# Performance work log

Hardware: AMD Instinct MI355X
Metric: run time of the kernel (lower is better)

Reference implementation:

```python
import jax, jax.numpy as jnp
import numpy as np

B, T, K = 128, 4096, 64
START, STOP = 62, 63
NEG = -10000.0


def setup_inputs() -> dict:
    key = jax.random.key(0)
    k1, k2, k3 = jax.random.split(key, 3)
    feats = jax.random.normal(k1, (B, T, K), dtype=jnp.float32)
    # gold tags never include START/STOP
    tags = jax.random.randint(k2, (B, T), 0, START)
    transitions = jax.random.normal(k3, (K, K), dtype=jnp.float32)
    # mirror the torch __init__ masking: no transition INTO start, none OUT of stop
    transitions = transitions.at[START, :].set(NEG).at[:, STOP].set(NEG)
    return {"feats": feats, "tags": tags, "transitions": transitions}


def _crf_single(feats, tags, transitions):
    """feats: [T,K], tags: [T], transitions: [K,K] (trans[next, prev])."""
    init = jnp.full((K,), NEG, dtype=feats.dtype).at[START].set(0.0)

    # ---- forward algorithm (log partition), vectorized over the tag loop ----
    def fwd_step(alpha, feat):
        # alpha[i] + trans[j, i] + feat[j]  ->  logsumexp over prev i
        new = jax.nn.logsumexp(alpha[None, :] + transitions, axis=1) + feat
        return new, None

    alpha, _ = jax.lax.scan(fwd_step, init, feats)
    forward_score = jax.nn.logsumexp(alpha + transitions[STOP])

    # ---- gold path score (_score_session) ----
    prev_tags = jnp.concatenate([jnp.array([START], dtype=tags.dtype), tags[:-1]])
    emit = jnp.take_along_axis(feats, tags[:, None], axis=1)[:, 0]  # feats[t, tags[t]]
    gold_score = jnp.sum(transitions[tags, prev_tags] + emit) + transitions[STOP, tags[-1]]

    nll = forward_score - gold_score  # neg_log_likelihood

    # ---- Viterbi decode ----
    def vit_step(delta, feat):
        scores = delta[None, :] + transitions  # [next, prev]
        bp = jnp.argmax(scores, axis=1)
        new = jnp.max(scores, axis=1) + feat  # feat added after argmax, as in torch
        return new, bp

    delta, bps = jax.lax.scan(vit_step, init, feats)  # bps: [T, K]
    terminal = delta + transitions[STOP]
    best_last = jnp.argmax(terminal)
    path_score = terminal[best_last]

    def back_step(tag, bp_t):
        return bp_t[tag], tag

    _, best_path = jax.lax.scan(back_step, best_last, bps, reverse=True)  # [T]
    return nll, path_score, best_path


def reference(feats, tags, transitions):
    nll, path_score, best_path = jax.vmap(_crf_single, in_axes=(0, 0, None))(
        feats, tags, transitions
    )
    return nll, path_score, best_path
```

## Files before the change

### kernel.cpp

```cpp
#include <hip/hip_runtime.h>

namespace {
constexpr int Tn = 4096;
constexpr int Kn = 64;
constexpr int BATCH = 128;
constexpr int START_TAG = 62;
constexpr int STOP_TAG = 63;
constexpr float NEGV = -10000.0f;
constexpr int CH = 64;
constexpr int NCH = Tn / CH;
constexpr int GL = 8;
constexpr int NG = Tn / GL;
constexpr int RS = 128;
constexpr int RB = 128;
constexpr int CW = 16;

__device__ __forceinline__ float rfl(float x) {
    return __uint_as_float(__builtin_amdgcn_readfirstlane(__float_as_uint(x)));
}
__device__ __forceinline__ void cfence() { __asm__ volatile("" ::: "memory"); }
__device__ __forceinline__ void lgkm0() { __asm__ volatile("s_waitcnt lgkmcnt(0)" ::: "memory"); }
__device__ __forceinline__ int imin(int a, int b) { return a < b ? a : b; }
__device__ __forceinline__ float m3(float a, float b, float c) {
    return fmaxf(fmaxf(a, b), c);
}

__global__ __launch_bounds__(256, 1)
void crf_kernel(const float* __restrict__ feats,
                const int* __restrict__ tags,
                const float* __restrict__ trans,
                float* __restrict__ out,
                unsigned int* __restrict__ bp32)
{
    const int tid = threadIdx.x;
    const int lane = tid & 63;
    const int wid = tid >> 6;
    const int b = blockIdx.x & (BATCH - 1);
    const size_t fb = (size_t)b * Tn * Kn;

    __shared__ float gw[4];
    __shared__ __align__(16) float vbuf[Kn];
    __shared__ __align__(16) float ring_v[RS][Kn];
    __shared__ float ring_m[RS][Kn];
    __shared__ unsigned char ring_bp[RB][Kn];
    __shared__ unsigned char snap[NCH * Kn];
    __shared__ unsigned char echain[NCH];
    __shared__ int prog_a[Kn], prog_b[Kn], prog_c[Kn], prog_d[Kn];
    __shared__ int done_b[Kn], done_c[Kn];

#define GATHER16(BASE) do {                                                    \
        const float4* vp_ = (const float4*)(BASE);                             \
        g0 = vp_[0];  g1 = vp_[1];  g2 = vp_[2];  g3 = vp_[3];                 \
        g4 = vp_[4];  g5 = vp_[5];  g6 = vp_[6];  g7 = vp_[7];                 \
        g8 = vp_[8];  g9 = vp_[9];  g10 = vp_[10]; g11 = vp_[11];              \
        g12 = vp_[12]; g13 = vp_[13]; g14 = vp_[14]; g15 = vp_[15];            \
    } while (0)

    if (blockIdx.x < BATCH) {
        float gold = 0.0f;
        {
            const int t0 = tid * (Tn / 256);
            int prev = (tid == 0) ? START_TAG : tags[(size_t)b * Tn + t0 - 1];
            for (int k = 0; k < Tn / 256; ++k) {
                const int t = t0 + k;
                const int tg = tags[(size_t)b * Tn + t];
                gold += trans[tg * Kn + prev] + feats[fb + (size_t)t * Kn + tg];
                prev = tg;
            }
            if (tid == 255) gold += trans[STOP_TAG * Kn + prev];
            #pragma unroll
            for (int off = 32; off; off >>= 1) gold += __shfl_down(gold, off);
            if (lane == 0) gw[wid] = gold;
        }
        __syncthreads();
        if (wid != 0) return;

        float ES[Kn];
        #pragma unroll
        for (int q = 0; q < Kn / 4; ++q) {
            const float4 t4 = ((const float4*)(trans + lane * Kn))[q];
            ES[4*q+0] = __expf(t4.x); ES[4*q+1] = __expf(t4.y);
            ES[4*q+2] = __expf(t4.z); ES[4*q+3] = __expf(t4.w);
        }
        float v = (lane == START_TAG) ? 1.0f : 0.0f;
        float O = 0.0f;
        float fc[GL], fn[GL], Fc[GL];
        #pragma unroll
        for (int k = 0; k < GL; ++k) fc[k] = feats[fb + (size_t)k * Kn + lane];

        float4 g0, g1, g2, g3, g4, g5, g6, g7, g8, g9, g10, g11, g12, g13, g14, g15;
        vbuf[lane] = v;
        GATHER16(vbuf);

#define FMAQ(Q, A, B2, C, D) ({                                                \
        float s0_ = 0.f, s1_ = 0.f, s2_ = 0.f, s3_ = 0.f;                      \
        s0_ = fmaf(ES[16*(Q)+0],  (A).x,  s0_); s1_ = fmaf(ES[16*(Q)+1],  (A).y,  s1_); \
        s2_ = fmaf(ES[16*(Q)+2],  (A).z,  s2_); s3_ = fmaf(ES[16*(Q)+3],  (A).w,  s3_); \
        s0_ = fmaf(ES[16*(Q)+4],  (B2).x, s0_); s1_ = fmaf(ES[16*(Q)+5],  (B2).y, s1_); \
        s2_ = fmaf(ES[16*(Q)+6],  (B2).z, s2_); s3_ = fmaf(ES[16*(Q)+7],  (B2).w, s3_); \
        s0_ = fmaf(ES[16*(Q)+8],  (C).x,  s0_); s1_ = fmaf(ES[16*(Q)+9],  (C).y,  s1_); \
        s2_ = fmaf(ES[16*(Q)+10], (C).z,  s2_); s3_ = fmaf(ES[16*(Q)+11], (C).w,  s3_); \
        s0_ = fmaf(ES[16*(Q)+12], (D).x,  s0_); s1_ = fmaf(ES[16*(Q)+13], (D).y,  s1_); \
        s2_ = fmaf(ES[16*(Q)+14], (D).z,  s2_); s3_ = fmaf(ES[16*(Q)+15], (D).w,  s3_); \
        (s0_ + s1_) + (s2_ + s3_); })

#define FWD_STEP(K) do {                                                       \
        const float w0_ = FMAQ(0, g0,  g1,  g2,  g3);                          \
        const float w1_ = FMAQ(1, g4,  g5,  g6,  g7);                          \
        const float w2_ = FMAQ(2, g8,  g9,  g10, g11);                         \
        const float w3_ = FMAQ(3, g12, g13, g14, g15);                         \
        const float w_ = ((w0_ + w1_) + (w2_ + w3_)) * Fc[K];                  \
        const float wz_ = rfl(w_);                                             \
        v = w_ * __builtin_amdgcn_rcpf(wz_);                                   \
        vbuf[lane] = v;                                                        \
        GATHER16(vbuf);                 \
        O += __logf(wz_);                   \
    } while (0)

        for (int g = 0; g < NG; ++g) {
            if (g + 1 < NG) {
                const size_t base = fb + (size_t)(g + 1) * GL * Kn + lane;
                #pragma unroll
                for (int k = 0; k < GL; ++k) fn[k] = feats[base + (size_t)k * Kn];
            }
            #pragma unroll
            for (int k = 0; k < GL; ++k) Fc[k] = __expf(fc[k]);
            #pragma unroll
            for (int k = 0; k < GL; ++k) FWD_STEP(k);
            #pragma unroll
            for (int k = 0; k < GL; ++k) fc[k] = fn[k];
        }
#undef FWD_STEP
        {
            const float a = O + __logf(v);
            const float x = a + trans[STOP_TAG * Kn + lane];
            float mx = x;
            #pragma unroll
            for (int off = 32; off; off >>= 1) mx = fmaxf(mx, __shfl_xor(mx, off));
            float se = __expf(x - mx);
            #pragma unroll
            for (int off = 32; off; off >>= 1) se += __shfl_xor(se, off);
            if (lane == 0)
                out[b] = (mx + __logf(se)) - (((gw[0] + gw[1]) + (gw[2] + gw[3])));
        }
        return;
    }

    volatile int* pa = (volatile int*)prog_a;
    volatile int* pb = (volatile int*)prog_b;
    volatile int* pc = (volatile int*)prog_c;
    volatile int* pd = (volatile int*)prog_d;
    volatile int* db = (volatile int*)done_b;
    volatile int* dc = (volatile int*)done_c;
    if (wid == 0) { pa[lane] = 0; pb[lane] = 0; }
    if (wid == 1) { pc[lane] = 0; pd[lane] = 0; }
    if (wid == 2) { db[lane] = 0; dc[lane] = 0; }
    __syncthreads();

    float trS[Kn];
    #pragma unroll
    for (int q = 0; q < Kn / 4; ++q) {
        const float4 t4 = ((const float4*)(trans + lane * Kn))[q];
        trS[4*q+0] = t4.x; trS[4*q+1] = t4.y; trS[4*q+2] = t4.z; trS[4*q+3] = t4.w;
    }

    if (wid == 0) {
        float v = (lane == START_TAG) ? 0.0f : NEGV;
        float fc[GL], fn[GL];
        #pragma unroll
        for (int k = 0; k < GL; ++k) fc[k] = feats[fb + (size_t)k * Kn + lane];

        float4 g0, g1, g2, g3, g4, g5, g6, g7, g8, g9, g10, g11, g12, g13, g14, g15;
        ring_v[0][lane] = v;
        GATHER16(ring_v[0]);

#define VQ(Q, DV) ({                                                           \
        const float sx_ = (DV).x + trS[4*(Q)+0];                               \
        const float sy_ = (DV).y + trS[4*(Q)+1];                               \
        const float sz_ = (DV).z + trS[4*(Q)+2];                               \
        const float sw_ = (DV).w + trS[4*(Q)+3];                               \
        fmaxf(m3(sx_, sy_, sz_), sw_); })

#define VIT_STEP(K) do {                                                       \
        const int t_ = g * GL + (K);                                           \
        const float q0_  = VQ(0,  g0),  q1_  = VQ(1,  g1);                     \
        const float q2_  = VQ(2,  g2),  q3_  = VQ(3,  g3);                     \
        const float q4_  = VQ(4,  g4),  q5_  = VQ(5,  g5);                     \
        const float q6_  = VQ(6,  g6),  q7_  = VQ(7,  g7);                     \
        const float q8_  = VQ(8,  g8),  q9_  = VQ(9,  g9);                     \
        const float q10_ = VQ(10, g10), q11_ = VQ(11, g11);                    \
        const float q12_ = VQ(12, g12), q13_ = VQ(13, g13);                    \
        const float q14_ = VQ(14, g14), q15_ = VQ(15, g15);                    \
        const float r0_ = m3(q0_,  q1_,  q2_);                                 \
        const float r1_ = m3(q3_,  q4_,  q5_);                                 \
        const float r2_ = m3(q6_,  q7_,  q8_);                                 \
        const float r3_ = m3(q9_,  q10_, q11_);                                \
        const float r4_ = m3(q12_, q13_, q14_);                                \
        const float mm_ = fmaxf(m3(m3(r0_, r1_, r2_), r3_, r4_), q15_);        \
        v = mm_ + fc[K];                 \
        float* nb_ = ring_v[(t_ + 1) & (RS - 1)];                              \
        nb_[lane] = v;                                                         \
        GATHER16(nb_);                   \
        ring_m[t_ & (RS - 1)][lane] = mm_;             \
    } while (0)

        for (int g = 0; g < NG; ++g) {
            if (g + 1 < NG) {
                const size_t base = fb + (size_t)(g + 1) * GL * Kn + lane;
                #pragma unroll
                for (int k = 0; k < GL; ++k) fn[k] = feats[base + (size_t)k * Kn];
            }
            if ((g & 3) == 0 && g >= 16) {
                const int t0 = g * GL;
                cfence();
                while (pb[lane] < t0 - 88 || pc[lane] < t0 - 88)
                    __builtin_amdgcn_s_sleep(1);
                cfence();
            }
            #pragma unroll
            for (int k = 0; k < GL; ++k) VIT_STEP(k);
            cfence();
            pa[lane] = g * GL + GL;
            #pragma unroll
            for (int k = 0; k < GL; ++k) fc[k] = fn[k];
        }
#undef VIT_STEP
#undef VQ
        const float term = v + trans[STOP_TAG * Kn + lane];
        float bv = term;
        int bi = lane;
        #pragma unroll
        for (int off = 32; off; off >>= 1) {
            const float ov = __shfl_xor(bv, off);
            const int oi = __shfl_xor(bi, off);
            if (ov > bv || (ov == bv && oi < bi)) { bv = ov; bi = oi; }
        }
        if (lane == 0) out[BATCH + b] = bv;
        while (pd[lane] < Tn) __builtin_amdgcn_s_sleep(1);
        cfence();
        if (lane == 0) {
            int e = bi;
            for (int c = NCH - 1; c >= 0; --c) {
                echain[c] = (unsigned char)e;
                e = snap[c * Kn + e];
            }
        }
        lgkm0();
        while (db[lane] == 0 || dc[lane] == 0) __builtin_amdgcn_s_sleep(1);
        cfence();
        int tag = echain[lane];
        float* po = out + 2 * BATCH + (size_t)b * Tn;
        const size_t dwb = (size_t)b * (Tn / 4);
        for (int k = CH - 1; k >= 0; --k) {
            const int t = lane * CH + k;
            po[t] = (float)tag;
            tag = (int)((bp32[(dwb + (size_t)(t >> 2)) * Kn + tag] >> (8 * (t & 3))) & 63u);
        }
    } else if (wid == 1 || wid == 2) {
        const int par = wid - 1;
        const size_t dwb = (size_t)b * (Tn / 4);
        volatile int* my = (par == 0) ? pb : pc;
        for (int c0 = par * CW; c0 < Tn; c0 += 2 * CW) {
            while (pa[lane] < c0 + CW) __builtin_amdgcn_s_sleep(1);
            cfence();
            if (c0 >= RB) {
                while (pd[lane] < c0 - (RB - CW)) __builtin_amdgcn_s_sleep(1);
                cfence();
            }
            for (int k4 = 0; k4 < CW; k4 += 4) {
                unsigned int bp4 = 0;
                #pragma unroll
                for (int k = 0; k < 4; ++k) {
                    const int t = c0 + k4 + k;
                    const float4* vp = (const float4*)ring_v[t & (RS - 1)];
                    const float m = ring_m[t & (RS - 1)][lane];
                    int qi[16];
                    #pragma unroll
                    for (int q = 0; q < 16; ++q) {
                        const float4 dv = vp[q];
                        const float sx = dv.x + trS[4*q+0];
                        const float sy = dv.y + trS[4*q+1];
                        const float sz = dv.z + trS[4*q+2];
                        const float sw = dv.w + trS[4*q+3];
                        const int ix = (sx == m) ? 4*q+0 : 255;
                        const int iy = (sy == m) ? 4*q+1 : 255;
                        const int iz = (sz == m) ? 4*q+2 : 255;
                        const int iw = (sw == m) ? 4*q+3 : 255;
                        qi[q] = imin(imin(ix, iy), imin(iz, iw));
                    }
                    int i8[8];
                    #pragma unroll
                    for (int q = 0; q < 8; ++q) i8[q] = imin(qi[2*q], qi[2*q+1]);
                    const int idx = imin(imin(imin(i8[0], i8[1]), imin(i8[2], i8[3])),
                                         imin(imin(i8[4], i8[5]), imin(i8[6], i8[7])));
                    ring_bp[t & (RB - 1)][lane] = (unsigned char)idx;
                    bp4 |= (unsigned int)idx << (8 * k);
                }
                bp32[(dwb + (size_t)((c0 + k4) >> 2)) * Kn + lane] = bp4;
            }
            cfence();
            my[lane] = c0 + CW;
        }
        __asm__ volatile("s_waitcnt vmcnt(0)" ::: "memory");
        if (par == 0) db[lane] = 1; else dc[lane] = 1;
    } else {
        int h = lane;
        for (int c0 = 0; c0 < Tn; c0 += CW) {
            volatile int* pp = ((c0 >> 4) & 1) ? pc : pb;
            while (pp[lane] < c0 + CW) __builtin_amdgcn_s_sleep(1);
            cfence();
            int bpv[CW];
            #pragma unroll
            for (int k = 0; k < CW; ++k)
                bpv[k] = (int)ring_bp[(c0 + k) & (RB - 1)][lane];
            #pragma unroll
            for (int k = 0; k < CW; ++k) h = __shfl(h, bpv[k]);
            if (((c0 >> 4) & 3) == 3) {
                snap[(c0 >> 6) * Kn + lane] = (unsigned char)h;
                h = lane;
            }
            cfence();
            pd[lane] = c0 + CW;
        }
    }
#undef GATHER16
#undef FMAQ
}
}

extern "C" void kernel_launch(void* const* d_in, const int* in_sizes, int n_in,
                              void* d_out, int out_size, void* d_ws, size_t ws_size,
                              hipStream_t stream)
{
    const float* feats = (const float*)d_in[0];
    const int* tags   = (const int*)d_in[1];
    const float* trans = (const float*)d_in[2];
    float* out = (float*)d_out;
    unsigned int* bp = (unsigned int*)d_ws;
    hipLaunchKernelGGL(crf_kernel, dim3(2 * BATCH), dim3(256), 0, stream,
                       feats, tags, trans, out, bp);
}
```

Before: 1.684 ms.

## Broadcast recurrence state via readlane and tree-compose backpointer shuffles

The forward and Viterbi recurrences no longer write the 64-wide state vector to LDS and read it back as 16 float4s each step. Each lane now pulls the previous-step values straight from registers with v_readlane, removing an LDS store/load round trip from the serial critical path; the price is 64 readlanes per step plus possible VALU-to-readlane hazard stalls. The backtrace wave also stops applying 16 chained shuffles to h. It composes the 16 backpointer maps in a pairwise tree first, so the serial shuffle chain is only a few levels deep. Viterbi still writes ring_v and ring_m for the other waves, and the ring_m store is moved earlier.

```diff
diff --git a/kernel.cpp b/kernel.cpp
--- a/kernel.cpp
+++ b/kernel.cpp
@@ -25,6 +25,8 @@
     return fmaxf(fmaxf(a, b), c);
 }
 
+#define RLV(I) __int_as_float(__builtin_amdgcn_readlane(vi_, (I)))
+
 __global__ __launch_bounds__(256, 1)
 void crf_kernel(const float* __restrict__ feats,
                 const int* __restrict__ tags,
@@ -39,22 +41,13 @@
     const size_t fb = (size_t)b * Tn * Kn;
 
     __shared__ float gw[4];
-    __shared__ __align__(16) float vbuf[Kn];
     __shared__ __align__(16) float ring_v[RS][Kn];
-    __shared__ float ring_m[RS][Kn];
+    __shared__ __align__(16) float ring_m[RS][Kn];
     __shared__ unsigned char ring_bp[RB][Kn];
     __shared__ unsigned char snap[NCH * Kn];
     __shared__ unsigned char echain[NCH];
     __shared__ int prog_a[Kn], prog_b[Kn], prog_c[Kn], prog_d[Kn];
     __shared__ int done_b[Kn], done_c[Kn];
-
-#define GATHER16(BASE) do {                                                    \
-        const float4* vp_ = (const float4*)(BASE);                             \
-        g0 = vp_[0];  g1 = vp_[1];  g2 = vp_[2];  g3 = vp_[3];                 \
-        g4 = vp_[4];  g5 = vp_[5];  g6 = vp_[6];  g7 = vp_[7];                 \
-        g8 = vp_[8];  g9 = vp_[9];  g10 = vp_[10]; g11 = vp_[11];              \
-        g12 = vp_[12]; g13 = vp_[13]; g14 = vp_[14]; g15 = vp_[15];            \
-    } while (0)
 
     if (blockIdx.x < BATCH) {
         float gold = 0.0f;
@@ -88,33 +81,36 @@
         #pragma unroll
         for (int k = 0; k < GL; ++k) fc[k] = feats[fb + (size_t)k * Kn + lane];
 
-        float4 g0, g1, g2, g3, g4, g5, g6, g7, g8, g9, g10, g11, g12, g13, g14, g15;
-        vbuf[lane] = v;
-        GATHER16(vbuf);
-
-#define FMAQ(Q, A, B2, C, D) ({                                                \
+#define FMAQ_RL(Q) ({                                                          \
         float s0_ = 0.f, s1_ = 0.f, s2_ = 0.f, s3_ = 0.f;                      \
-        s0_ = fmaf(ES[16*(Q)+0],  (A).x,  s0_); s1_ = fmaf(ES[16*(Q)+1],  (A).y,  s1_); \
-        s2_ = fmaf(ES[16*(Q)+2],  (A).z,  s2_); s3_ = fmaf(ES[16*(Q)+3],  (A).w,  s3_); \
-        s0_ = fmaf(ES[16*(Q)+4],  (B2).x, s0_); s1_ = fmaf(ES[16*(Q)+5],  (B2).y, s1_); \
-        s2_ = fmaf(ES[16*(Q)+6],  (B2).z, s2_); s3_ = fmaf(ES[16*(Q)+7],  (B2).w, s3_); \
-        s0_ = fmaf(ES[16*(Q)+8],  (C).x,  s0_); s1_ = fmaf(ES[16*(Q)+9],  (C).y,  s1_); \
-        s2_ = fmaf(ES[16*(Q)+10], (C).z,  s2_); s3_ = fmaf(ES[16*(Q)+11], (C).w,  s3_); \
-        s0_ = fmaf(ES[16*(Q)+12], (D).x,  s0_); s1_ = fmaf(ES[16*(Q)+13], (D).y,  s1_); \
-        s2_ = fmaf(ES[16*(Q)+14], (D).z,  s2_); s3_ = fmaf(ES[16*(Q)+15], (D).w,  s3_); \
+        s0_ = fmaf(ES[16*(Q)+0],  RLV(16*(Q)+0),  s0_);                        \
+        s1_ = fmaf(ES[16*(Q)+1],  RLV(16*(Q)+1),  s1_);                        \
+        s2_ = fmaf(ES[16*(Q)+2],  RLV(16*(Q)+2),  s2_);                        \
+        s3_ = fmaf(ES[16*(Q)+3],  RLV(16*(Q)+3),  s3_);                        \
+        s0_ = fmaf(ES[16*(Q)+4],  RLV(16*(Q)+4),  s0_);                        \
+        s1_ = fmaf(ES[16*(Q)+5],  RLV(16*(Q)+5),  s1_);                        \
+        s2_ = fmaf(ES[16*(Q)+6],  RLV(16*(Q)+6),  s2_);                        \
+        s3_ = fmaf(ES[16*(Q)+7],  RLV(16*(Q)+7),  s3_);                        \
+        s0_ = fmaf(ES[16*(Q)+8],  RLV(16*(Q)+8),  s0_);                        \
+        s1_ = fmaf(ES[16*(Q)+9],  RLV(16*(Q)+9),  s1_);                        \
+        s2_ = fmaf(ES[16*(Q)+10], RLV(16*(Q)+10), s2_);                        \
+        s3_ = fmaf(ES[16*(Q)+11], RLV(16*(Q)+11), s3_);                        \
+        s0_ = fmaf(ES[16*(Q)+12], RLV(16*(Q)+12), s0_);                        \
+        s1_ = fmaf(ES[16*(Q)+13], RLV(16*(Q)+13), s1_);                        \
+        s2_ = fmaf(ES[16*(Q)+14], RLV(16*(Q)+14), s2_);                        \
+        s3_ = fmaf(ES[16*(Q)+15], RLV(16*(Q)+15), s3_);                        \
         (s0_ + s1_) + (s2_ + s3_); })
 
 #define FWD_STEP(K) do {                                                       \
-        const float w0_ = FMAQ(0, g0,  g1,  g2,  g3);                          \
-        const float w1_ = FMAQ(1, g4,  g5,  g6,  g7);                          \
-        const float w2_ = FMAQ(2, g8,  g9,  g10, g11);                         \
-        const float w3_ = FMAQ(3, g12, g13, g14, g15);                         \
+        const int vi_ = __float_as_int(v);                                     \
+        const float w0_ = FMAQ_RL(0);                                          \
+        const float w1_ = FMAQ_RL(1);                                          \
+        const float w2_ = FMAQ_RL(2);                                          \
+        const float w3_ = FMAQ_RL(3);                                          \
         const float w_ = ((w0_ + w1_) + (w2_ + w3_)) * Fc[K];                  \
         const float wz_ = rfl(w_);                                             \
         v = w_ * __builtin_amdgcn_rcpf(wz_);                                   \
-        vbuf[lane] = v;                                                        \
-        GATHER16(vbuf);                 \
-        O += __logf(wz_);                   \
+        O += __logf(wz_);                                                      \
     } while (0)
 
         for (int g = 0; g < NG; ++g) {
@@ -170,38 +166,35 @@
         #pragma unroll
         for (int k = 0; k < GL; ++k) fc[k] = feats[fb + (size_t)k * Kn + lane];
 
-        float4 g0, g1, g2, g3, g4, g5, g6, g7, g8, g9, g10, g11, g12, g13, g14, g15;
         ring_v[0][lane] = v;
-        GATHER16(ring_v[0]);
-
-#define VQ(Q, DV) ({                                                           \
-        const float sx_ = (DV).x + trS[4*(Q)+0];                               \
-        const float sy_ = (DV).y + trS[4*(Q)+1];                               \
-        const float sz_ = (DV).z + trS[4*(Q)+2];                               \
-        const float sw_ = (DV).w + trS[4*(Q)+3];                               \
+
+#define VQ_RL(Q) ({                                                            \
+        const float sx_ = RLV(4*(Q)+0) + trS[4*(Q)+0];                         \
+        const float sy_ = RLV(4*(Q)+1) + trS[4*(Q)+1];                         \
+        const float sz_ = RLV(4*(Q)+2) + trS[4*(Q)+2];                         \
+        const float sw_ = RLV(4*(Q)+3) + trS[4*(Q)+3];                         \
         fmaxf(m3(sx_, sy_, sz_), sw_); })
 
 #define VIT_STEP(K) do {                                                       \
         const int t_ = g * GL + (K);                                           \
-        const float q0_  = VQ(0,  g0),  q1_  = VQ(1,  g1);                     \
-        const float q2_  = VQ(2,  g2),  q3_  = VQ(3,  g3);                     \
-        const float q4_  = VQ(4,  g4),  q5_  = VQ(5,  g5);                     \
-        const float q6_  = VQ(6,  g6),  q7_  = VQ(7,  g7);                     \
-        const float q8_  = VQ(8,  g8),  q9_  = VQ(9,  g9);                     \
-        const float q10_ = VQ(10, g10), q11_ = VQ(11, g11);                    \
-        const float q12_ = VQ(12, g12), q13_ = VQ(13, g13);                    \
-        const float q14_ = VQ(14, g14), q15_ = VQ(15, g15);                    \
+        const int vi_ = __float_as_int(v);                                     \
+        const float q0_  = VQ_RL(0),  q1_  = VQ_RL(1);                         \
+        const float q2_  = VQ_RL(2),  q3_  = VQ_RL(3);                         \
+        const float q4_  = VQ_RL(4),  q5_  = VQ_RL(5);                         \
+        const float q6_  = VQ_RL(6),  q7_  = VQ_RL(7);                         \
+        const float q8_  = VQ_RL(8),  q9_  = VQ_RL(9);                         \
+        const float q10_ = VQ_RL(10), q11_ = VQ_RL(11);                        \
+        const float q12_ = VQ_RL(12), q13_ = VQ_RL(13);                        \
+        const float q14_ = VQ_RL(14), q15_ = VQ_RL(15);                        \
         const float r0_ = m3(q0_,  q1_,  q2_);                                 \
         const float r1_ = m3(q3_,  q4_,  q5_);                                 \
         const float r2_ = m3(q6_,  q7_,  q8_);                                 \
         const float r3_ = m3(q9_,  q10_, q11_);                                \
         const float r4_ = m3(q12_, q13_, q14_);                                \
         const float mm_ = fmaxf(m3(m3(r0_, r1_, r2_), r3_, r4_), q15_);        \
+        ring_m[t_ & (RS - 1)][lane] = mm_;        \
         v = mm_ + fc[K];                 \
-        float* nb_ = ring_v[(t_ + 1) & (RS - 1)];                              \
-        nb_[lane] = v;                                                         \
-        GATHER16(nb_);                   \
-        ring_m[t_ & (RS - 1)][lane] = mm_;             \
+        ring_v[(t_ + 1) & (RS - 1)][lane] = v;                                 \
     } while (0)
 
         for (int g = 0; g < NG; ++g) {
@@ -225,7 +218,7 @@
             for (int k = 0; k < GL; ++k) fc[k] = fn[k];
         }
 #undef VIT_STEP
-#undef VQ
+#undef VQ_RL
         const float term = v + trans[STOP_TAG * Kn + lane];
         float bv = term;
         int bi = lane;
@@ -313,8 +306,15 @@
             #pragma unroll
             for (int k = 0; k < CW; ++k)
                 bpv[k] = (int)ring_bp[(c0 + k) & (RB - 1)][lane];
-            #pragma unroll
-            for (int k = 0; k < CW; ++k) h = __shfl(h, bpv[k]);
+            const int p0 = __shfl(bpv[0],  bpv[1]),  p1 = __shfl(bpv[2],  bpv[3]);
+            const int p2 = __shfl(bpv[4],  bpv[5]),  p3 = __shfl(bpv[6],  bpv[7]);
+            const int p4 = __shfl(bpv[8],  bpv[9]),  p5 = __shfl(bpv[10], bpv[11]);
+            const int p6 = __shfl(bpv[12], bpv[13]), p7 = __shfl(bpv[14], bpv[15]);
+            const int q0 = __shfl(p0, p1), q1 = __shfl(p2, p3);
+            const int q2 = __shfl(p4, p5), q3 = __shfl(p6, p7);
+            const int r0 = __shfl(q0, q1), r1 = __shfl(q2, q3);
+            const int C = __shfl(r0, r1);
+            h = __shfl(h, C);
             if (((c0 >> 4) & 3) == 3) {
                 snap[(c0 >> 6) * Kn + lane] = (unsigned char)h;
                 h = lane;
@@ -323,8 +323,7 @@
             pd[lane] = c0 + CW;
         }
     }
-#undef GATHER16
-#undef FMAQ
+#undef FMAQ_RL
 }
 }
 
```

Result: slower. 2.121 ms (+26.0%).
